# Optimization experiments

Hardware: AMD Instinct MI355X
Metric: run time of the kernel (lower is better)

The kernel has to match this reference:

```python
import jax, jax.numpy as jnp
import numpy as np


def setup_inputs() -> dict:
    key = jax.random.key(0)
    k1, k2, k3, k4, k5 = jax.random.split(key, 5)
    n_mol, n_atm, d_feat, n_props = 128, 64, 384, 64
    n_ref = n_mol * n_atm  # 8192 reference atoms (flattened)
    # element labels in {1,2,3,4} (e.g. H,C,N,O); all atoms nondummy (Z>0)
    Z_ref = jax.random.randint(k1, (n_mol, n_atm), 1, 5)
    Z = jax.random.randint(k2, (n_mol, n_atm), 1, 5)
    # descriptors, scaled so the poly kernel K^expK stays O(1)
    scale = 1.0 / np.sqrt(d_feat).astype(np.float32)
    X_ref = jax.random.normal(k3, (n_ref, d_feat), jnp.float32) * scale
    desc = jax.random.normal(k4, (n_mol, n_atm, d_feat), jnp.float32) * scale
    Alpha = jax.random.normal(k5, (n_props, n_ref), jnp.float32)
    return {"Alpha": Alpha, "X_ref": X_ref, "desc": desc,
            "Z_ref": Z_ref, "Z": Z, "expK": 2}


def reference(Alpha, X_ref, desc, Z_ref, Z, expK):
    # Faithful dense formulation of the per-element gather/matmul/scatter:
    # y[p, j] = sum_i Alpha[p, i] * (X_ref[i] . X_in[j])^expK * [Z_ref[i] == Z[j]]
    # Each query atom j belongs to exactly one element, so the masked dense
    # kernel reproduces the grouped computation exactly (same flat ordering
    # as torch's molecule-major concatenation).
    d_feat = X_ref.shape[-1]
    X_in = desc.reshape(-1, d_feat)                      # [N_in, d]
    K = jnp.power(X_ref @ X_in.T, expK)                  # [N_ref, N_in]
    mask = Z_ref.reshape(-1)[:, None] == Z.reshape(-1)[None, :]
    y = Alpha @ jnp.where(mask, K, jnp.float32(0.0))     # [n_props, N_in]
    return y
```

## Files before the change

### kernel.cpp

```cpp
#include <hip/hip_runtime.h>
#include <hip/hip_bf16.h>
#include <stdint.h>


typedef __attribute__((ext_vector_type(8))) short bf16x8;
typedef __attribute__((ext_vector_type(4))) float f32x4;
typedef __attribute__((ext_vector_type(4))) unsigned int u32x4;

#define DFEAT  384
#define NREF   8192
#define NIN    8192
#define NPROPS 64
#define BJ 128
#define BI 128
#define BK 32
#define KSTEPS (DFEAT / BK)
#define CAP    8704
#define NSTRIP (CAP / BJ)

__device__ __forceinline__ void gload_lds16(const void* g, void* l) {
  __builtin_amdgcn_global_load_lds(
      (const __attribute__((address_space(1))) void*)g,
      (__attribute__((address_space(3))) void*)l,
      16, 0, 0);
}

__device__ __forceinline__ unsigned short bfbits(float f) {
  __hip_bfloat16 h = __float2bfloat16(f);
  return __builtin_bit_cast(unsigned short, h);
}

__device__ __forceinline__ float pwr(float s, int expK) {
  if (expK == 2) return s * s;
  float r = 1.0f;
  for (int e = 0; e < expK; ++e) r *= s;
  return r;
}

__global__ __launch_bounds__(256) void partition2_kernel(
    const int* __restrict__ Za, const int* __restrict__ Zb,
    int* __restrict__ perma, int* __restrict__ permb,
    int* __restrict__ goffa, int* __restrict__ goffb) {
  const int* Zin = blockIdx.x ? Zb : Za;
  int* perm = blockIdx.x ? permb : perma;
  int* goff = blockIdx.x ? goffb : goffa;

  __shared__ int cnt[256][4];
  __shared__ int gstart[4];
  __shared__ int gtot[4];
  const int t = threadIdx.x;
  const int base = t * 32;

  int c[4] = {0, 0, 0, 0};
  int zloc[32];
  #pragma unroll
  for (int e = 0; e < 32; ++e) {
    zloc[e] = (Zin[base + e] - 1) & 3;
    ++c[zloc[e]];
  }
  #pragma unroll
  for (int b = 0; b < 4; ++b) cnt[t][b] = c[b];
  __syncthreads();

  const int w = t >> 6, l = t & 63;
  {
    int v0 = cnt[4 * l + 0][w], v1 = cnt[4 * l + 1][w];
    int v2 = cnt[4 * l + 2][w], v3 = cnt[4 * l + 3][w];
    int s = v0 + v1 + v2 + v3;
    int inc = s;
    #pragma unroll
    for (int d = 1; d < 64; d <<= 1) {
      int o = __shfl_up(inc, d, 64);
      if (l >= d) inc += o;
    }
    const int excl = inc - s;
    cnt[4 * l + 0][w] = excl;
    cnt[4 * l + 1][w] = excl + v0;
    cnt[4 * l + 2][w] = excl + v0 + v1;
    cnt[4 * l + 3][w] = excl + v0 + v1 + v2;
    if (l == 63) gtot[w] = inc;
  }
  __syncthreads();

  if (t == 0) {
    int off = 0;
    #pragma unroll
    for (int b = 0; b < 4; ++b) {
      gstart[b] = off; goff[b] = off;
      off += ((gtot[b] + 127) >> 7) << 7;
    }
    goff[4] = off;
  }
  __syncthreads();

  for (int s = t; s < CAP; s += 256) perm[s] = -1;
  __syncthreads();

  int pos[4];
  #pragma unroll
  for (int b = 0; b < 4; ++b) pos[b] = gstart[b] + cnt[t][b];
  #pragma unroll
  for (int e = 0; e < 32; ++e) {
    const int z = zloc[e];
    perm[pos[z]++] = base + e;
  }
}

#define XSEC (CAP * (DFEAT / 4) / 256)
__global__ void gather_all(const float* __restrict__ Xr_in,
                           const float* __restrict__ Xi_in,
                           const float* __restrict__ Al_in,
                           const int* __restrict__ perm_i,
                           const int* __restrict__ perm_j,
                           __hip_bfloat16* __restrict__ Xr_g,
                           __hip_bfloat16* __restrict__ Xi_g,
                           __hip_bfloat16* __restrict__ Ab_g) {
  const int b = blockIdx.x;
  if (b < 2 * XSEC) {
    const bool isA = (b < XSEC);
    const float* in = isA ? Xr_in : Xi_in;
    const int* perm = isA ? perm_i : perm_j;
    __hip_bfloat16* out = isA ? Xr_g : Xi_g;
    const int idx = (isA ? b : b - XSEC) * 256 + threadIdx.x;
    const int per_row = DFEAT / 4;
    const int slot = idx / per_row;
    const int c4 = (idx % per_row) * 4;
    const int src = perm[slot];
    ushort4 o = make_ushort4(0, 0, 0, 0);
    if (src >= 0) {
      float4 v = *reinterpret_cast<const float4*>(in + (size_t)src * DFEAT + c4);
      o.x = bfbits(v.x); o.y = bfbits(v.y); o.z = bfbits(v.z); o.w = bfbits(v.w);
    }
    *reinterpret_cast<ushort4*>(out + (size_t)slot * DFEAT + c4) = o;
  } else {
    const int t = (b - 2 * XSEC) * 256 + threadIdx.x;
    const int per_row = CAP / 4;
    const int p  = t / per_row;
    const int c4 = t % per_row;
    const int blk = c4 >> 3;
    const int g   = c4 & 7;
    const int l4g = g >> 1;
    const int eh  = g & 1;
    ushort4 o;
    unsigned short* op = &o.x;
    #pragma unroll
    for (int r = 0; r < 4; ++r) {
      const int slot = blk * 32 + eh * 16 + l4g * 4 + r;
      const int src = perm_i[slot];
      op[r] = (src >= 0) ? bfbits(Al_in[(size_t)p * NREF + src]) : (unsigned short)0;
    }
    *reinterpret_cast<ushort4*>(Ab_g + (size_t)p * CAP + blk * 32 + l4g * 8 + eh * 4) = o;
  }
}

__global__ void reduce_scatter(const float* __restrict__ partial,
                               const int* __restrict__ permj,
                               float* __restrict__ out, int nsplit) {
  const int idx = blockIdx.x * blockDim.x + threadIdx.x;
  const int per_row = CAP / 4;
  const int p = idx / per_row;
  const int s4 = (idx % per_row) * 4;
  float4 s = make_float4(0.f, 0.f, 0.f, 0.f);
  for (int sp = 0; sp < nsplit; ++sp) {
    float4 v = *reinterpret_cast<const float4*>(
        partial + (size_t)sp * NPROPS * CAP + (size_t)p * CAP + s4);
    s.x += v.x; s.y += v.y; s.z += v.z; s.w += v.w;
  }
  const int4 dst = *reinterpret_cast<const int4*>(permj + s4);
  float* po = out + (size_t)p * NIN;
  if (dst.x >= 0) po[dst.x] = s.x;
  if (dst.y >= 0) po[dst.y] = s.y;
  if (dst.z >= 0) po[dst.z] = s.z;
  if (dst.w >= 0) po[dst.w] = s.w;
}

__global__ __launch_bounds__(256, 2) void fused_poly_kernel(
    const __hip_bfloat16* __restrict__ Xr,
    const __hip_bfloat16* __restrict__ Xi,
    const __hip_bfloat16* __restrict__ Abp,
    const int* __restrict__ ioff,
    const int* __restrict__ joff,
    const int* __restrict__ expKp,
    float* __restrict__ partial,
    int nsplit, int chunk)
{
  const int flat = blockIdx.x;
  const int newflat = (flat & 7) * chunk + (flat >> 3);
  const int strip = newflat / nsplit;
  const int split = newflat % nsplit;
  const int j0 = strip * BJ;
  if (j0 >= joff[4]) return;

  int grp = 0;
  grp += (j0 >= joff[1]);
  grp += (j0 >= joff[2]);
  grp += (j0 >= joff[3]);
  const int ibase = ioff[grp];
  const int ntiles_g = (ioff[grp + 1] - ibase) / BI;
  const int tb = ntiles_g / nsplit;
  const int rem = ntiles_g % nsplit;
  const int ntiles = tb + (split < rem ? 1 : 0);
  const int tile_begin = split * tb + (split < rem ? split : rem);

  const int tid  = threadIdx.x;
  const int wid  = tid >> 6;
  const int lane = tid & 63;
  const int l15  = lane & 15;
  const int l4   = lane >> 4;
  const int wi   = wid >> 1;
  const int wj   = wid & 1;

  __shared__ char smem[49152];

  const int expK = *expKp;

  const int rsl = (l4 ^ ((l15 >> 1) & 3)) << 4;
  const int scol = ((lane & 3) ^ ((lane >> 3) & 3)) * 8;
  const int srow = lane >> 2;

  auto stage = [&](int buf, int i0s, int kks) {
    char* Ab_ = smem + buf * 16384;
    char* Bb_ = smem + buf * 16384 + 8192;
    #pragma unroll
    for (int q = 0; q < 2; ++q) {
      const int grow = wid * 32 + q * 16 + srow;
      const size_t gc = (size_t)kks * BK + scol;
      gload_lds16(Xr + (size_t)(i0s + grow) * DFEAT + gc,
                  Ab_ + wid * 2048 + q * 1024);
      gload_lds16(Xi + (size_t)(j0 + grow) * DFEAT + gc,
                  Bb_ + wid * 2048 + q * 1024);
    }
  };

  f32x4 accO[4][4];
  #pragma unroll
  for (int a = 0; a < 4; ++a)
    #pragma unroll
    for (int n = 0; n < 4; ++n)
      accO[a][n] = (f32x4){0.f, 0.f, 0.f, 0.f};

  if (ntiles > 0) {
    stage(0, ibase + tile_begin * BI, 0);
    stage(1, ibase + tile_begin * BI, 1);

    for (int t = 0; t < ntiles; ++t) {
      const int i0c = ibase + (tile_begin + t) * BI;
      const int i0n = i0c + BI;

      f32x4 acc[4][4];
      #pragma unroll
      for (int m = 0; m < 4; ++m)
        #pragma unroll
        for (int n = 0; n < 4; ++n)
          acc[m][n] = (f32x4){0.f, 0.f, 0.f, 0.f};

      #pragma unroll
      for (int ph = 0; ph < KSTEPS; ++ph) {
        const int cb = ph % 3;
        const int sb = (ph + 2) % 3;
        if (ph <= 9) {
          stage(sb, i0c, ph + 2);
          asm volatile("s_waitcnt vmcnt(8)" ::: "memory");
        } else if (t + 1 < ntiles) {
          stage(sb, i0n, ph - 10);
          asm volatile("s_waitcnt vmcnt(8)" ::: "memory");
        } else if (ph == 10) {
          asm volatile("s_waitcnt vmcnt(4)" ::: "memory");
        } else {
          asm volatile("s_waitcnt vmcnt(0)" ::: "memory");
        }
        __builtin_amdgcn_s_barrier();

        char* Ab_ = smem + cb * 16384;
        char* Bb_ = smem + cb * 16384 + 8192;
        __builtin_amdgcn_s_setprio(1);
        {
          bf16x8 aF[4], bF[4];
          #pragma unroll
          for (int m = 0; m < 4; ++m) {
            const int rA = wi * 64 + m * 16 + l15;
            aF[m] = *reinterpret_cast<const bf16x8*>(Ab_ + rA * 64 + rsl);
          }
          #pragma unroll
          for (int n = 0; n < 4; ++n) {
            const int rB = wj * 64 + n * 16 + l15;
            bF[n] = *reinterpret_cast<const bf16x8*>(Bb_ + rB * 64 + rsl);
          }
          #pragma unroll
          for (int m = 0; m < 4; ++m)
            #pragma unroll
            for (int n = 0; n < 4; ++n)
              acc[m][n] = __builtin_amdgcn_mfma_f32_16x16x32_bf16(
                  aF[m], bF[n], acc[m][n], 0, 0, 0);
        }
        __builtin_amdgcn_s_setprio(0);
        asm volatile("s_waitcnt lgkmcnt(0)" ::: "memory");
        __builtin_amdgcn_s_barrier();
      }

      #pragma unroll
      for (int ks = 0; ks < 2; ++ks) {
        bf16x8 aP[4];
        #pragma unroll
        for (int a = 0; a < 4; ++a)
          aP[a] = *reinterpret_cast<const bf16x8*>(
              Abp + (size_t)(a * 16 + l15) * CAP + i0c + wi * 64 + ks * 32 + l4 * 8);
        #pragma unroll
        for (int n = 0; n < 4; ++n) {
          const f32x4 s0 = acc[2 * ks][n];
          const f32x4 s1 = acc[2 * ks + 1][n];
          u32x4 tw;
          tw[0] = (uint32_t)bfbits(pwr(s0[0], expK)) |
                  ((uint32_t)bfbits(pwr(s0[1], expK)) << 16);
          tw[1] = (uint32_t)bfbits(pwr(s0[2], expK)) |
                  ((uint32_t)bfbits(pwr(s0[3], expK)) << 16);
          tw[2] = (uint32_t)bfbits(pwr(s1[0], expK)) |
                  ((uint32_t)bfbits(pwr(s1[1], expK)) << 16);
          tw[3] = (uint32_t)bfbits(pwr(s1[2], expK)) |
                  ((uint32_t)bfbits(pwr(s1[3], expK)) << 16);
          const bf16x8 bP = __builtin_bit_cast(bf16x8, tw);
          __builtin_amdgcn_s_setprio(1);
          #pragma unroll
          for (int a = 0; a < 4; ++a)
            accO[a][n] = __builtin_amdgcn_mfma_f32_16x16x32_bf16(
                aP[a], bP, accO[a][n], 0, 0, 0);
          __builtin_amdgcn_s_setprio(0);
        }
      }
    }
  }

  __syncthreads();
  float* rb = (float*)smem;
  if (wi == 1) {
    #pragma unroll
    for (int a = 0; a < 4; ++a)
      #pragma unroll
      for (int n = 0; n < 4; ++n)
        #pragma unroll
        for (int r = 0; r < 4; ++r)
          rb[wj * 4096 + (a * 16 + l4 * 4 + r) * 64 + n * 16 + l15] =
              accO[a][n][r];
  }
  __syncthreads();
  if (wi == 0) {
    float* po = partial + (size_t)split * NPROPS * CAP;
    #pragma unroll
    for (int a = 0; a < 4; ++a)
      #pragma unroll
      for (int n = 0; n < 4; ++n)
        #pragma unroll
        for (int r = 0; r < 4; ++r) {
          const int p = a * 16 + l4 * 4 + r;
          const int jl = wj * 64 + n * 16 + l15;
          po[(size_t)p * CAP + j0 + jl] =
              accO[a][n][r] + rb[wj * 4096 + p * 64 + n * 16 + l15];
        }
  }
}

extern "C" void kernel_launch(void* const* d_in, const int* in_sizes, int n_in,
                              void* d_out, int out_size, void* d_ws, size_t ws_size,
                              hipStream_t stream) {
  (void)in_sizes; (void)n_in; (void)out_size;
  const float* Alpha = (const float*)d_in[0];
  const float* X_ref = (const float*)d_in[1];
  const float* desc  = (const float*)d_in[2];
  const int*   Z_ref = (const int*)d_in[3];
  const int*   Z     = (const int*)d_in[4];
  const int*   expK  = (const int*)d_in[5];
  float* out = (float*)d_out;

  char* ws = (char*)d_ws;
  size_t off = 0;
  auto alloc = [&](size_t b) { void* p = ws + off; off = (off + b + 255) & ~255ULL; return p; };

  int* perm_i = (int*)alloc(CAP * 4);
  int* perm_j = (int*)alloc(CAP * 4);
  int* ioff   = (int*)alloc(8 * 4);
  int* joff   = (int*)alloc(8 * 4);
  __hip_bfloat16* Xr_g = (__hip_bfloat16*)alloc((size_t)CAP * DFEAT * 2);
  __hip_bfloat16* Xi_g = (__hip_bfloat16*)alloc((size_t)CAP * DFEAT * 2);
  __hip_bfloat16* Ab_g = (__hip_bfloat16*)alloc((size_t)NPROPS * CAP * 2);

  int nsplit = 12;
  while (nsplit > 4 && off + (size_t)nsplit * NPROPS * CAP * 4 > ws_size) nsplit -= 4;
  float* partial = (float*)alloc((size_t)nsplit * NPROPS * CAP * 4);

  partition2_kernel<<<dim3(2), 256, 0, stream>>>(
      Z_ref, Z, perm_i, perm_j, ioff, joff);

  gather_all<<<dim3(2 * XSEC + NPROPS * (CAP / 4) / 256), 256, 0, stream>>>(
      X_ref, desc, Alpha, perm_i, perm_j, Xr_g, Xi_g, Ab_g);

  const int grid = NSTRIP * nsplit;
  fused_poly_kernel<<<dim3(grid), 256, 0, stream>>>(
      Xr_g, Xi_g, Ab_g, ioff, joff, expK, partial, nsplit, grid / 8);

  reduce_scatter<<<dim3(NPROPS * (CAP / 4) / 256), 256, 0, stream>>>(
      partial, perm_j, out, nsplit);
}
```

Measured before the change: 69.58 us.

## Fuse split-K reduction and scatter into the last-arriving block per strip

Drops the separate reduce_scatter kernel. Each fused_poly block now bumps a per-strip atomic counter after writing its partial tile. The last block to finish a strip sums all nsplit partials for that strip and scatters them through perm_j to the output. This removes one kernel launch and its tail, and lets the reduction overlap with other strips still computing, at the cost of thread fences, an atomic per block, and a serial reduction inside one block per strip.

```diff
diff --git a/kernel.cpp b/kernel.cpp
--- a/kernel.cpp
+++ b/kernel.cpp
@@ -40,7 +40,8 @@
 __global__ __launch_bounds__(256) void partition2_kernel(
     const int* __restrict__ Za, const int* __restrict__ Zb,
     int* __restrict__ perma, int* __restrict__ permb,
-    int* __restrict__ goffa, int* __restrict__ goffb) {
+    int* __restrict__ goffa, int* __restrict__ goffb,
+    int* __restrict__ strip_cnt) {
   const int* Zin = blockIdx.x ? Zb : Za;
   int* perm = blockIdx.x ? permb : perma;
   int* goff = blockIdx.x ? goffb : goffa;
@@ -50,6 +51,8 @@
   __shared__ int gtot[4];
   const int t = threadIdx.x;
   const int base = t * 32;
+
+  if (blockIdx.x == 0 && t < NSTRIP) strip_cnt[t] = 0;
 
   int c[4] = {0, 0, 0, 0};
   int zloc[32];
@@ -153,27 +156,6 @@
   }
 }
 
-__global__ void reduce_scatter(const float* __restrict__ partial,
-                               const int* __restrict__ permj,
-                               float* __restrict__ out, int nsplit) {
-  const int idx = blockIdx.x * blockDim.x + threadIdx.x;
-  const int per_row = CAP / 4;
-  const int p = idx / per_row;
-  const int s4 = (idx % per_row) * 4;
-  float4 s = make_float4(0.f, 0.f, 0.f, 0.f);
-  for (int sp = 0; sp < nsplit; ++sp) {
-    float4 v = *reinterpret_cast<const float4*>(
-        partial + (size_t)sp * NPROPS * CAP + (size_t)p * CAP + s4);
-    s.x += v.x; s.y += v.y; s.z += v.z; s.w += v.w;
-  }
-  const int4 dst = *reinterpret_cast<const int4*>(permj + s4);
-  float* po = out + (size_t)p * NIN;
-  if (dst.x >= 0) po[dst.x] = s.x;
-  if (dst.y >= 0) po[dst.y] = s.y;
-  if (dst.z >= 0) po[dst.z] = s.z;
-  if (dst.w >= 0) po[dst.w] = s.w;
-}
-
 __global__ __launch_bounds__(256, 2) void fused_poly_kernel(
     const __hip_bfloat16* __restrict__ Xr,
     const __hip_bfloat16* __restrict__ Xi,
@@ -182,6 +164,9 @@
     const int* __restrict__ joff,
     const int* __restrict__ expKp,
     float* __restrict__ partial,
+    const int* __restrict__ permj,
+    float* __restrict__ outp,
+    int* __restrict__ strip_cnt,
     int nsplit, int chunk)
 {
   const int flat = blockIdx.x;
@@ -211,6 +196,7 @@
   const int wj   = wid & 1;
 
   __shared__ char smem[49152];
+  __shared__ int elect;
 
   const int expK = *expKp;
 
@@ -357,6 +343,30 @@
               accO[a][n][r] + rb[wj * 4096 + p * 64 + n * 16 + l15];
         }
   }
+
+  __threadfence();
+  __syncthreads();
+  if (tid == 0) elect = atomicAdd(&strip_cnt[strip], 1);
+  __syncthreads();
+  if (elect == nsplit - 1) {
+    __threadfence();
+    for (int v = tid; v < NPROPS * (BJ / 4); v += 256) {
+      const int p  = v >> 5;
+      const int jq = (v & 31) * 4;
+      float4 s = make_float4(0.f, 0.f, 0.f, 0.f);
+      for (int sp = 0; sp < nsplit; ++sp) {
+        const float4 x = *reinterpret_cast<const float4*>(
+            partial + (size_t)sp * NPROPS * CAP + (size_t)p * CAP + j0 + jq);
+        s.x += x.x; s.y += x.y; s.z += x.z; s.w += x.w;
+      }
+      const int4 dst = *reinterpret_cast<const int4*>(permj + j0 + jq);
+      float* po = outp + (size_t)p * NIN;
+      if (dst.x >= 0) po[dst.x] = s.x;
+      if (dst.y >= 0) po[dst.y] = s.y;
+      if (dst.z >= 0) po[dst.z] = s.z;
+      if (dst.w >= 0) po[dst.w] = s.w;
+    }
+  }
 }
 
 extern "C" void kernel_launch(void* const* d_in, const int* in_sizes, int n_in,
@@ -379,6 +389,7 @@
   int* perm_j = (int*)alloc(CAP * 4);
   int* ioff   = (int*)alloc(8 * 4);
   int* joff   = (int*)alloc(8 * 4);
+  int* scnt   = (int*)alloc(NSTRIP * 4);
   __hip_bfloat16* Xr_g = (__hip_bfloat16*)alloc((size_t)CAP * DFEAT * 2);
   __hip_bfloat16* Xi_g = (__hip_bfloat16*)alloc((size_t)CAP * DFEAT * 2);
   __hip_bfloat16* Ab_g = (__hip_bfloat16*)alloc((size_t)NPROPS * CAP * 2);
@@ -388,15 +399,13 @@
   float* partial = (float*)alloc((size_t)nsplit * NPROPS * CAP * 4);
 
   partition2_kernel<<<dim3(2), 256, 0, stream>>>(
-      Z_ref, Z, perm_i, perm_j, ioff, joff);
+      Z_ref, Z, perm_i, perm_j, ioff, joff, scnt);
 
   gather_all<<<dim3(2 * XSEC + NPROPS * (CAP / 4) / 256), 256, 0, stream>>>(
       X_ref, desc, Alpha, perm_i, perm_j, Xr_g, Xi_g, Ab_g);
 
   const int grid = NSTRIP * nsplit;
   fused_poly_kernel<<<dim3(grid), 256, 0, stream>>>(
-      Xr_g, Xi_g, Ab_g, ioff, joff, expK, partial, nsplit, grid / 8);
-
-  reduce_scatter<<<dim3(NPROPS * (CAP / 4) / 256), 256, 0, stream>>>(
-      partial, perm_j, out, nsplit);
-}
+      Xr_g, Xi_g, Ab_g, ioff, joff, expK, partial, perm_j, out, scnt,
+      nsplit, grid / 8);
+}
```

Result: slower. 210.4 us (+202.4%).
